# Kernel optimization log

Hardware: AMD Instinct MI355X
Metric: run time of the kernel (lower is better)

The kernel has to match this reference:

```python
import jax, jax.numpy as jnp
import numpy as np

NEARZERO = 1e-5
NMUL = 16
NSTEP = 365
NGRID = 10000

# change_param_range: lb + raw * (ub - lb)
HBV_BOUNDS = {'parBETA': (1.0, 6.0), 'parK0': (0.05, 0.9), 'parBETAET': (0.3, 5.0)}
WL_BOUNDS = {'parFC': (50.0, 1000.0), 'parK1': (0.01, 0.5), 'parK2': (0.001, 0.2),
             'parLP': (0.2, 1.0), 'parPERC': (0.0, 10.0), 'parUZL': (0.0, 100.0),
             'parTT': (-2.5, 2.5), 'parCFMAX': (0.5, 10.0), 'parCFR': (0.0, 0.1),
             'parCWH': (0.0, 0.2), 'parC': (0.0, 1.0), 'parTRbound': (0.0, 20.0),
             'parAc': (0.0, 2500.0)}


def setup_inputs() -> dict:
    key = jax.random.key(0)
    kP, kT, kE, kp, kw, ka = jax.random.split(key, 6)
    P = jax.random.uniform(kP, (NSTEP, NGRID)) * 20.0          # precip [mm/day]
    T = jax.random.uniform(kT, (NSTEP, NGRID)) * 30.0 - 5.0    # temp [C]
    PET = jax.random.uniform(kE, (NSTEP, NGRID)) * 6.0         # PET [mm/day]
    x_hydro_model = jnp.stack([P, T, PET], axis=-1)            # [Nstep, Ngrid, 3]
    params_raw = jax.random.uniform(kp, (NSTEP, NGRID, 3, NMUL))
    waterloss_params_raw = jax.random.uniform(kw, (NGRID, 13, NMUL))
    ac_batch = jax.random.uniform(ka, (NGRID,)) * 3000.0       # drainage area proxy
    return {'x_hydro_model': x_hydro_model, 'params_raw': params_raw,
            'waterloss_params_raw': waterloss_params_raw, 'ac_batch': ac_batch}


def _scale_params(params_raw, waterloss_params_raw, static_idx=-1):
    p = {}
    for i, (name, (lb, ub)) in enumerate(HBV_BOUNDS.items()):
        p[name] = lb + params_raw[static_idx, :, i, :] * (ub - lb)       # [Ngrid, nmul]
    for i, (name, (lb, ub)) in enumerate(WL_BOUNDS.items()):
        p[name] = lb + waterloss_params_raw[:, i, :] * (ub - lb)         # [Ngrid, nmul]
    return p


def reference(x_hydro_model, params_raw, waterloss_params_raw, ac_batch):
    p = _scale_params(params_raw, waterloss_params_raw)
    P = x_hydro_model[:, :, 0]
    T = x_hydro_model[:, :, 1]
    PET = x_hydro_model[:, :, 2]

    acm = jnp.broadcast_to(ac_batch[:, None], (NGRID, NMUL))
    # regional flow is time-invariant (static params, static ac)
    rf = jnp.clip((acm - p['parAc']) / 1000.0, -1.0, 1.0)
    regional_flow = (rf * p['parTRbound'] * (acm < 2500.0).astype(rf.dtype)
                     + jnp.exp(jnp.clip(-(acm - 2500.0) / 50.0, -10.0, 0.0))
                       * p['parTRbound'] * (acm >= 2500.0).astype(rf.dtype))

    init_state = tuple(jnp.full((NGRID, NMUL), 0.001, dtype=jnp.float32) for _ in range(5))

    def step(carry, xs):
        SNOWPACK, MELTWATER, SM, SUZ, SLZ = carry
        Pt, Tt, PETt = xs
        Pm = Pt[:, None]
        Tm = Tt[:, None]
        PETm = PETt[:, None]
        warm = (Tm >= p['parTT']).astype(Pm.dtype)
        RAIN = Pm * warm
        SNOW = Pm * (1.0 - warm)
        SNOWPACK = SNOWPACK + SNOW
        melt = jnp.minimum(jnp.maximum(p['parCFMAX'] * (Tm - p['parTT']), 0.0), SNOWPACK)
        MELTWATER = MELTWATER + melt
        SNOWPACK = SNOWPACK - melt
        refreezing = jnp.minimum(
            jnp.maximum(p['parCFR'] * p['parCFMAX'] * (p['parTT'] - Tm), 0.0), MELTWATER)
        SNOWPACK = SNOWPACK + refreezing
        MELTWATER = MELTWATER - refreezing
        tosoil = jnp.maximum(MELTWATER - p['parCWH'] * SNOWPACK, 0.0)
        MELTWATER = MELTWATER - tosoil
        soil_wetness = jnp.clip((SM / p['parFC']) ** p['parBETA'], 0.0, 1.0)
        recharge = (RAIN + tosoil) * soil_wetness
        SM = SM + RAIN + tosoil - recharge
        excess = jnp.maximum(SM - p['parFC'], 0.0)
        SM = SM - excess
        evapfactor = jnp.clip((SM / (p['parLP'] * p['parFC'])) ** p['parBETAET'], 0.0, 1.0)
        ETact = jnp.minimum(SM, PETm * evapfactor)
        SM = jnp.maximum(SM - ETact, NEARZERO)
        capillary = jnp.minimum(SLZ, p['parC'] * SLZ * (1.0 - jnp.minimum(SM / p['parFC'], 1.0)))
        SM = jnp.maximum(SM + capillary, NEARZERO)
        SLZ = jnp.maximum(SLZ - capillary, NEARZERO)
        SUZ = SUZ + recharge + excess
        PERC = jnp.minimum(SUZ, p['parPERC'])
        SUZ = SUZ - PERC
        Q0 = p['parK0'] * jnp.maximum(SUZ - p['parUZL'], 0.0)
        SUZ = SUZ - Q0
        Q1 = p['parK1'] * SUZ
        SUZ = SUZ - Q1
        SLZ = SLZ + PERC
        SLZ = jnp.maximum(SLZ + regional_flow, 0.0)
        Q2 = p['parK2'] * SLZ
        SLZ = SLZ - Q2
        q = (Q0 + Q1 + Q2).mean(-1)  # Qsimavg over nmul components -> [Ngrid]
        return (SNOWPACK, MELTWATER, SM, SUZ, SLZ), q

    _, Qsimavg = jax.lax.scan(step, init_state, (P, T, PET))  # [Nstep, Ngrid]
    return Qsimavg
```

## Files before the change

### kernel.cpp

```cpp
#include <hip/hip_runtime.h>

#define NMUL 16
#define NSTEP 365
#define NGRID 10000
#define NEARZERO 1e-5f


__device__ __forceinline__ float fast_pow(float x, float y) {
    return __expf(y * __logf(x));
}

__global__ __launch_bounds__(256) void hbv_kernel(
    const float* __restrict__ x,
    const float* __restrict__ pr,
    const float* __restrict__ wl,
    const float* __restrict__ ac,
    float* __restrict__ out)
{
    const int tid = blockIdx.x * blockDim.x + threadIdx.x;
    const int g = tid >> 4;
    const int m = tid & 15;
    if (g >= NGRID) return;

    const size_t pbase = ((size_t)(NSTEP - 1) * NGRID + (size_t)g) * 3 * NMUL + (size_t)m;
    const float parBETA   = 1.0f  + pr[pbase + 0 * NMUL] * 5.0f;
    const float parK0     = 0.05f + pr[pbase + 1 * NMUL] * 0.85f;
    const float parBETAET = 0.3f  + pr[pbase + 2 * NMUL] * 4.7f;

    const size_t wbase = (size_t)g * 13 * NMUL + (size_t)m;
    const float parFC    = 50.0f  + wl[wbase +  0 * NMUL] * 950.0f;
    const float parK1    = 0.01f  + wl[wbase +  1 * NMUL] * 0.49f;
    const float parK2    = 0.001f + wl[wbase +  2 * NMUL] * 0.199f;
    const float parLP    = 0.2f   + wl[wbase +  3 * NMUL] * 0.8f;
    const float parPERC  =          wl[wbase +  4 * NMUL] * 10.0f;
    const float parUZL   =          wl[wbase +  5 * NMUL] * 100.0f;
    const float parTT    = -2.5f  + wl[wbase +  6 * NMUL] * 5.0f;
    const float parCFMAX = 0.5f   + wl[wbase +  7 * NMUL] * 9.5f;
    const float parCFR   =          wl[wbase +  8 * NMUL] * 0.1f;
    const float parCWH   =          wl[wbase +  9 * NMUL] * 0.2f;
    const float parC     =          wl[wbase + 10 * NMUL] * 1.0f;
    const float parTR    =          wl[wbase + 11 * NMUL] * 20.0f;
    const float parAc    =          wl[wbase + 12 * NMUL] * 2500.0f;

    const float acm = ac[g];
    float regional_flow;
    if (acm < 2500.0f) {
        float rf = fminf(fmaxf((acm - parAc) * 0.001f, -1.0f), 1.0f);
        regional_flow = rf * parTR;
    } else {
        float e = fminf(fmaxf(-(acm - 2500.0f) * 0.02f, -10.0f), 0.0f);
        regional_flow = __expf(e) * parTR;
    }

    const float invFC   = 1.0f / parFC;
    const float invLPFC = 1.0f / (parLP * parFC);
    const float CFRCFMAX = parCFR * parCFMAX;

    float SNOWPACK = 0.001f, MELTWATER = 0.001f, SM = 0.001f, SUZ = 0.001f, SLZ = 0.001f;

    for (int t = 0; t < NSTEP; ++t) {
        const size_t xi = ((size_t)t * NGRID + (size_t)g) * 3;
        const float Pm   = x[xi + 0];
        const float Tm   = x[xi + 1];
        const float PETm = x[xi + 2];

        const float warm = (Tm >= parTT) ? 1.0f : 0.0f;
        const float RAIN = Pm * warm;
        const float SNOW = Pm - RAIN;
        SNOWPACK += SNOW;
        const float melt = fminf(fmaxf(parCFMAX * (Tm - parTT), 0.0f), SNOWPACK);
        MELTWATER += melt;
        SNOWPACK  -= melt;
        const float refreezing = fminf(fmaxf(CFRCFMAX * (parTT - Tm), 0.0f), MELTWATER);
        SNOWPACK  += refreezing;
        MELTWATER -= refreezing;
        const float tosoil = fmaxf(MELTWATER - parCWH * SNOWPACK, 0.0f);
        MELTWATER -= tosoil;

        const float soil_wetness = fminf(fmaxf(fast_pow(SM * invFC, parBETA), 0.0f), 1.0f);
        const float recharge = (RAIN + tosoil) * soil_wetness;
        SM = SM + RAIN + tosoil - recharge;
        const float excess = fmaxf(SM - parFC, 0.0f);
        SM -= excess;
        const float evapfactor = fminf(fmaxf(fast_pow(SM * invLPFC, parBETAET), 0.0f), 1.0f);
        const float ETact = fminf(SM, PETm * evapfactor);
        SM = fmaxf(SM - ETact, NEARZERO);
        const float capillary = fminf(SLZ, parC * SLZ * (1.0f - fminf(SM * invFC, 1.0f)));
        SM  = fmaxf(SM + capillary, NEARZERO);
        SLZ = fmaxf(SLZ - capillary, NEARZERO);

        SUZ = SUZ + recharge + excess;
        const float PERCa = fminf(SUZ, parPERC);
        SUZ -= PERCa;
        const float Q0 = parK0 * fmaxf(SUZ - parUZL, 0.0f);
        SUZ -= Q0;
        const float Q1 = parK1 * SUZ;
        SUZ -= Q1;
        SLZ += PERCa;
        SLZ = fmaxf(SLZ + regional_flow, 0.0f);
        const float Q2 = parK2 * SLZ;
        SLZ -= Q2;

        float q = Q0 + Q1 + Q2;
        q += __shfl_xor(q, 1, 16);
        q += __shfl_xor(q, 2, 16);
        q += __shfl_xor(q, 4, 16);
        q += __shfl_xor(q, 8, 16);
        if (m == 0) {
            out[(size_t)t * NGRID + (size_t)g] = q * 0.0625f;
        }
    }
}

extern "C" void kernel_launch(void* const* d_in, const int* in_sizes, int n_in,
                              void* d_out, int out_size, void* d_ws, size_t ws_size,
                              hipStream_t stream) {
    const float* x  = (const float*)d_in[0];
    const float* pr = (const float*)d_in[1];
    const float* wl = (const float*)d_in[2];
    const float* ac = (const float*)d_in[3];
    float* out = (float*)d_out;

    const int total = NGRID * NMUL;
    const int block = 256;
    const int grid = (total + block - 1) / block;
    hbv_kernel<<<grid, block, 0, stream>>>(x, pr, wl, ac, out);
}
```

Before: 1.013 ms.

## Software-pipeline forcing loads and batch shuffle reductions over unrolled timesteps

Restructures the time loop into blocks of four steps. Forcing inputs for the next block are prefetched into registers while the current block computes, which hides global load latency behind the serial recurrence. The shuffle reductions for four steps are interleaved so they can issue together, and the redundant fmaxf(.,0) clamps on the pow results are dropped. The grid-bounds early return is also removed; this is safe only because NGRID*NMUL divides evenly by the block size. The cost is higher register pressure.

```diff
diff --git a/kernel.cpp b/kernel.cpp
--- a/kernel.cpp
+++ b/kernel.cpp
@@ -4,10 +4,62 @@
 #define NSTEP 365
 #define NGRID 10000
 #define NEARZERO 1e-5f
+#define UNROLL 4
 
 
 __device__ __forceinline__ float fast_pow(float x, float y) {
     return __expf(y * __logf(x));
+}
+
+struct HbvP {
+    float parBETA, parK0, parBETAET;
+    float parFC, parK1, parK2, parLP, parPERC, parUZL, parTT,
+          parCFMAX, parCWH, parC;
+    float invFC, invLPFC, CFRCFMAX, regional_flow;
+};
+
+__device__ __forceinline__ float hbv_step(
+    float Pm, float Tm, float PETm,
+    float& SNOWPACK, float& MELTWATER, float& SM, float& SUZ, float& SLZ,
+    const HbvP& p)
+{
+    const float RAIN = (Tm >= p.parTT) ? Pm : 0.0f;
+    const float SNOW = Pm - RAIN;
+    SNOWPACK += SNOW;
+    const float melt = fminf(fmaxf(p.parCFMAX * (Tm - p.parTT), 0.0f), SNOWPACK);
+    MELTWATER += melt;
+    SNOWPACK  -= melt;
+    const float refreezing = fminf(fmaxf(p.CFRCFMAX * (p.parTT - Tm), 0.0f), MELTWATER);
+    SNOWPACK  += refreezing;
+    MELTWATER -= refreezing;
+    const float tosoil = fmaxf(MELTWATER - p.parCWH * SNOWPACK, 0.0f);
+    MELTWATER -= tosoil;
+
+    const float soil_wetness = fminf(fast_pow(SM * p.invFC, p.parBETA), 1.0f);
+    const float recharge = (RAIN + tosoil) * soil_wetness;
+    SM = SM + RAIN + tosoil - recharge;
+    const float excess = fmaxf(SM - p.parFC, 0.0f);
+    SM -= excess;
+    const float evapfactor = fminf(fast_pow(SM * p.invLPFC, p.parBETAET), 1.0f);
+    const float ETact = fminf(SM, PETm * evapfactor);
+    SM = fmaxf(SM - ETact, NEARZERO);
+    const float capillary = fminf(SLZ, p.parC * SLZ * (1.0f - fminf(SM * p.invFC, 1.0f)));
+    SM  = fmaxf(SM + capillary, NEARZERO);
+    SLZ = fmaxf(SLZ - capillary, NEARZERO);
+
+    SUZ = SUZ + recharge + excess;
+    const float PERCa = fminf(SUZ, p.parPERC);
+    SUZ -= PERCa;
+    const float Q0 = p.parK0 * fmaxf(SUZ - p.parUZL, 0.0f);
+    SUZ -= Q0;
+    const float Q1 = p.parK1 * SUZ;
+    SUZ -= Q1;
+    SLZ += PERCa;
+    SLZ = fmaxf(SLZ + p.regional_flow, 0.0f);
+    const float Q2 = p.parK2 * SLZ;
+    SLZ -= Q2;
+
+    return Q0 + Q1 + Q2;
 }
 
 __global__ __launch_bounds__(256) void hbv_kernel(
@@ -20,95 +72,94 @@
     const int tid = blockIdx.x * blockDim.x + threadIdx.x;
     const int g = tid >> 4;
     const int m = tid & 15;
-    if (g >= NGRID) return;
 
+    HbvP p;
     const size_t pbase = ((size_t)(NSTEP - 1) * NGRID + (size_t)g) * 3 * NMUL + (size_t)m;
-    const float parBETA   = 1.0f  + pr[pbase + 0 * NMUL] * 5.0f;
-    const float parK0     = 0.05f + pr[pbase + 1 * NMUL] * 0.85f;
-    const float parBETAET = 0.3f  + pr[pbase + 2 * NMUL] * 4.7f;
+    p.parBETA   = 1.0f  + pr[pbase + 0 * NMUL] * 5.0f;
+    p.parK0     = 0.05f + pr[pbase + 1 * NMUL] * 0.85f;
+    p.parBETAET = 0.3f  + pr[pbase + 2 * NMUL] * 4.7f;
 
     const size_t wbase = (size_t)g * 13 * NMUL + (size_t)m;
-    const float parFC    = 50.0f  + wl[wbase +  0 * NMUL] * 950.0f;
-    const float parK1    = 0.01f  + wl[wbase +  1 * NMUL] * 0.49f;
-    const float parK2    = 0.001f + wl[wbase +  2 * NMUL] * 0.199f;
-    const float parLP    = 0.2f   + wl[wbase +  3 * NMUL] * 0.8f;
-    const float parPERC  =          wl[wbase +  4 * NMUL] * 10.0f;
-    const float parUZL   =          wl[wbase +  5 * NMUL] * 100.0f;
-    const float parTT    = -2.5f  + wl[wbase +  6 * NMUL] * 5.0f;
-    const float parCFMAX = 0.5f   + wl[wbase +  7 * NMUL] * 9.5f;
-    const float parCFR   =          wl[wbase +  8 * NMUL] * 0.1f;
-    const float parCWH   =          wl[wbase +  9 * NMUL] * 0.2f;
-    const float parC     =          wl[wbase + 10 * NMUL] * 1.0f;
-    const float parTR    =          wl[wbase + 11 * NMUL] * 20.0f;
-    const float parAc    =          wl[wbase + 12 * NMUL] * 2500.0f;
+    p.parFC    = 50.0f  + wl[wbase +  0 * NMUL] * 950.0f;
+    p.parK1    = 0.01f  + wl[wbase +  1 * NMUL] * 0.49f;
+    p.parK2    = 0.001f + wl[wbase +  2 * NMUL] * 0.199f;
+    p.parLP    = 0.2f   + wl[wbase +  3 * NMUL] * 0.8f;
+    p.parPERC  =          wl[wbase +  4 * NMUL] * 10.0f;
+    p.parUZL   =          wl[wbase +  5 * NMUL] * 100.0f;
+    p.parTT    = -2.5f  + wl[wbase +  6 * NMUL] * 5.0f;
+    p.parCFMAX = 0.5f   + wl[wbase +  7 * NMUL] * 9.5f;
+    const float parCFR =  wl[wbase +  8 * NMUL] * 0.1f;
+    p.parCWH   =          wl[wbase +  9 * NMUL] * 0.2f;
+    p.parC     =          wl[wbase + 10 * NMUL] * 1.0f;
+    const float parTR  =  wl[wbase + 11 * NMUL] * 20.0f;
+    const float parAc  =  wl[wbase + 12 * NMUL] * 2500.0f;
 
     const float acm = ac[g];
-    float regional_flow;
     if (acm < 2500.0f) {
         float rf = fminf(fmaxf((acm - parAc) * 0.001f, -1.0f), 1.0f);
-        regional_flow = rf * parTR;
+        p.regional_flow = rf * parTR;
     } else {
         float e = fminf(fmaxf(-(acm - 2500.0f) * 0.02f, -10.0f), 0.0f);
-        regional_flow = __expf(e) * parTR;
+        p.regional_flow = __expf(e) * parTR;
     }
 
-    const float invFC   = 1.0f / parFC;
-    const float invLPFC = 1.0f / (parLP * parFC);
-    const float CFRCFMAX = parCFR * parCFMAX;
+    p.invFC    = 1.0f / p.parFC;
+    p.invLPFC  = 1.0f / (p.parLP * p.parFC);
+    p.CFRCFMAX = parCFR * p.parCFMAX;
 
     float SNOWPACK = 0.001f, MELTWATER = 0.001f, SM = 0.001f, SUZ = 0.001f, SLZ = 0.001f;
 
-    for (int t = 0; t < NSTEP; ++t) {
-        const size_t xi = ((size_t)t * NGRID + (size_t)g) * 3;
-        const float Pm   = x[xi + 0];
-        const float Tm   = x[xi + 1];
-        const float PETm = x[xi + 2];
+    float P0[UNROLL], T0[UNROLL], E0[UNROLL];
+    #pragma unroll
+    for (int u = 0; u < UNROLL; ++u) {
+        const size_t xi = ((size_t)u * NGRID + (size_t)g) * 3;
+        P0[u] = x[xi + 0]; T0[u] = x[xi + 1]; E0[u] = x[xi + 2];
+    }
 
-        const float warm = (Tm >= parTT) ? 1.0f : 0.0f;
-        const float RAIN = Pm * warm;
-        const float SNOW = Pm - RAIN;
-        SNOWPACK += SNOW;
-        const float melt = fminf(fmaxf(parCFMAX * (Tm - parTT), 0.0f), SNOWPACK);
-        MELTWATER += melt;
-        SNOWPACK  -= melt;
-        const float refreezing = fminf(fmaxf(CFRCFMAX * (parTT - Tm), 0.0f), MELTWATER);
-        SNOWPACK  += refreezing;
-        MELTWATER -= refreezing;
-        const float tosoil = fmaxf(MELTWATER - parCWH * SNOWPACK, 0.0f);
-        MELTWATER -= tosoil;
+    int t = 0;
+    for (int blk = 0; blk < 91; ++blk) {
+        float P1[UNROLL], T1[UNROLL], E1[UNROLL];
+        const int tn = t + UNROLL;
+        if (blk < 90) {
+            #pragma unroll
+            for (int u = 0; u < UNROLL; ++u) {
+                const size_t xi = ((size_t)(tn + u) * NGRID + (size_t)g) * 3;
+                P1[u] = x[xi + 0]; T1[u] = x[xi + 1]; E1[u] = x[xi + 2];
+            }
+        } else {
+            #pragma unroll
+            for (int u = 0; u < UNROLL; ++u) { P1[u] = 0.f; T1[u] = 0.f; E1[u] = 0.f; }
+        }
 
-        const float soil_wetness = fminf(fmaxf(fast_pow(SM * invFC, parBETA), 0.0f), 1.0f);
-        const float recharge = (RAIN + tosoil) * soil_wetness;
-        SM = SM + RAIN + tosoil - recharge;
-        const float excess = fmaxf(SM - parFC, 0.0f);
-        SM -= excess;
-        const float evapfactor = fminf(fmaxf(fast_pow(SM * invLPFC, parBETAET), 0.0f), 1.0f);
-        const float ETact = fminf(SM, PETm * evapfactor);
-        SM = fmaxf(SM - ETact, NEARZERO);
-        const float capillary = fminf(SLZ, parC * SLZ * (1.0f - fminf(SM * invFC, 1.0f)));
-        SM  = fmaxf(SM + capillary, NEARZERO);
-        SLZ = fmaxf(SLZ - capillary, NEARZERO);
+        float q[UNROLL];
+        #pragma unroll
+        for (int u = 0; u < UNROLL; ++u)
+            q[u] = hbv_step(P0[u], T0[u], E0[u], SNOWPACK, MELTWATER, SM, SUZ, SLZ, p);
 
-        SUZ = SUZ + recharge + excess;
-        const float PERCa = fminf(SUZ, parPERC);
-        SUZ -= PERCa;
-        const float Q0 = parK0 * fmaxf(SUZ - parUZL, 0.0f);
-        SUZ -= Q0;
-        const float Q1 = parK1 * SUZ;
-        SUZ -= Q1;
-        SLZ += PERCa;
-        SLZ = fmaxf(SLZ + regional_flow, 0.0f);
-        const float Q2 = parK2 * SLZ;
-        SLZ -= Q2;
+        #pragma unroll
+        for (int s = 1; s < 16; s <<= 1) {
+            #pragma unroll
+            for (int u = 0; u < UNROLL; ++u)
+                q[u] += __shfl_xor(q[u], s, 16);
+        }
+        if (m == 0) {
+            #pragma unroll
+            for (int u = 0; u < UNROLL; ++u)
+                out[(size_t)(t + u) * NGRID + (size_t)g] = q[u] * 0.0625f;
+        }
 
-        float q = Q0 + Q1 + Q2;
-        q += __shfl_xor(q, 1, 16);
-        q += __shfl_xor(q, 2, 16);
-        q += __shfl_xor(q, 4, 16);
-        q += __shfl_xor(q, 8, 16);
-        if (m == 0) {
-            out[(size_t)t * NGRID + (size_t)g] = q * 0.0625f;
-        }
+        #pragma unroll
+        for (int u = 0; u < UNROLL; ++u) { P0[u] = P1[u]; T0[u] = T1[u]; E0[u] = E1[u]; }
+        t = tn;
+    }
+
+    {
+        const size_t xi = ((size_t)(NSTEP - 1) * NGRID + (size_t)g) * 3;
+        float q = hbv_step(x[xi + 0], x[xi + 1], x[xi + 2],
+                           SNOWPACK, MELTWATER, SM, SUZ, SLZ, p);
+        #pragma unroll
+        for (int s = 1; s < 16; s <<= 1) q += __shfl_xor(q, s, 16);
+        if (m == 0) out[(size_t)(NSTEP - 1) * NGRID + (size_t)g] = q * 0.0625f;
     }
 }
 
```

Result: faster. 947.6 us (-6.5%).
